# Kernel tuning notes

Hardware: AMD Instinct MI355X
Metric: run time of the kernel (lower is better)

The kernel has to match this reference:

```python
import jax, jax.numpy as jnp
import numpy as np

EPS = 1e-7      # GENConv message epsilon
BN_EPS = 1e-5   # torch BatchNorm1d eps


def _genconv(x, src, dst, n, w1, b1, gamma, beta, w2, b2):
    # GENConv(aggr='softmax_sg', t=1.0): msg = relu(x_j)+eps, per-feature
    # scatter-softmax weights (stop-grad), weighted sum, residual, MLP
    # [Linear -> BatchNorm(train stats) -> ReLU -> Linear].
    msg = jnp.maximum(x[src], 0.0) + EPS                         # [E, d]
    m = jax.ops.segment_max(msg, dst, num_segments=n)            # [N, d]
    e = jnp.exp(msg - m[dst])
    s = jax.ops.segment_sum(e, dst, num_segments=n)
    alpha = jax.lax.stop_gradient(e / (s[dst] + 1e-16))          # softmax_sg
    agg = jax.ops.segment_sum(msg * alpha, dst, num_segments=n)  # [N, d]
    h = agg + x
    h = h @ w1 + b1
    mu = jnp.mean(h, axis=0)
    var = jnp.var(h, axis=0)
    h = (h - mu) * jax.lax.rsqrt(var + BN_EPS) * gamma + beta
    h = jnp.maximum(h, 0.0)
    return h @ w2 + b2


def _forward(x, edge_index, batch, target,
             g1_w1, g1_b1, g1_g, g1_be, g1_w2, g1_b2,
             g2_w1, g2_b1, g2_g, g2_be, g2_w2, g2_b2,
             g3_w1, g3_b1, g3_g, g3_be, g3_w2, g3_b2,
             fg1_w, fg1_b, fg2_w, fg2_b, fg3_w, fg3_b,
             emb, cw, cb, fxt_w, fxt_b,
             f1_w, f1_b, f2_w, f2_b, o_w, o_b):
    n = x.shape[0]
    nb = target.shape[0]
    src, dst = edge_index[0], edge_index[1]
    h = jnp.maximum(_genconv(x, src, dst, n, g1_w1, g1_b1, g1_g, g1_be, g1_w2, g1_b2), 0.0)
    h = jnp.maximum(_genconv(h, src, dst, n, g2_w1, g2_b1, g2_g, g2_be, g2_w2, g2_b2), 0.0)
    h = jnp.maximum(_genconv(h, src, dst, n, g3_w1, g3_b1, g3_g, g3_be, g3_w2, g3_b2), 0.0)
    # global mean pool over graphs
    sums = jax.ops.segment_sum(h, batch, num_segments=nb)
    cnt = jax.ops.segment_sum(jnp.ones((n, 1), h.dtype), batch, num_segments=nb)
    xg = sums / jnp.maximum(cnt, 1.0)
    xg = jnp.maximum(xg @ fg1_w + fg1_b, 0.0)
    xg = jnp.maximum(xg @ fg2_w + fg2_b, 0.0)
    xg = jnp.maximum(xg @ fg3_w + fg3_b, 0.0)
    # protein branch: embed [B,1000,128], Conv1d(1000->32,k=8) over embed axis
    ext = emb[target]                                            # [B, 1000, 128]
    conv = jax.lax.conv_general_dilated(
        ext, cw, (1,), 'VALID',
        dimension_numbers=('NCW', 'OIW', 'NCW')) + cb[None, :, None]  # [B, 32, 121]
    xt = conv.reshape(nb, 32 * 121) @ fxt_w + fxt_b
    xc = jnp.concatenate([xg, xt], axis=1)                       # [B, 256]
    xc = jnp.maximum(xc @ f1_w + f1_b, 0.0)
    xc = jnp.maximum(xc @ f2_w + f2_b, 0.0)
    return xc @ o_w + o_b


def _lin(k, i, o):
    kw, kb = jax.random.split(k)
    s = 1.0 / np.sqrt(i)
    return (jax.random.uniform(kw, (i, o), jnp.float32, -s, s),
            jax.random.uniform(kb, (o,), jnp.float32, -s, s))


def setup_inputs():
    key = jax.random.key(0)
    ks = jax.random.split(key, 32)
    N, E, B, D = 30000, 150000, 256, 78
    d = {}
    d['x'] = jax.random.normal(ks[0], (N, D), jnp.float32)
    d['edge_index'] = jax.random.randint(ks[1], (2, E), 0, N)
    d['batch'] = jnp.sort(jax.random.randint(ks[2], (N,), 0, B))
    d['target'] = jax.random.randint(ks[3], (B, 1000), 0, 26)
    dims = [(78, 156, 78), (78, 156, 312), (312, 624, 624)]
    for li, (i, hdim, o) in enumerate(dims, start=1):
        w1, b1 = _lin(ks[4 + 2 * li], i, hdim)
        w2, b2 = _lin(ks[5 + 2 * li], hdim, o)
        d['g%d_w1' % li], d['g%d_b1' % li] = w1, b1
        d['g%d_g' % li] = jnp.ones((hdim,), jnp.float32)
        d['g%d_be' % li] = jnp.zeros((hdim,), jnp.float32)
        d['g%d_w2' % li], d['g%d_b2' % li] = w2, b2
    d['fg1_w'], d['fg1_b'] = _lin(ks[14], 624, 512)
    d['fg2_w'], d['fg2_b'] = _lin(ks[15], 512, 1024)
    d['fg3_w'], d['fg3_b'] = _lin(ks[16], 1024, 128)
    d['emb'] = jax.random.normal(ks[17], (26, 128), jnp.float32)
    s = 1.0 / np.sqrt(1000 * 8)
    d['cw'] = jax.random.uniform(ks[18], (32, 1000, 8), jnp.float32, -s, s)
    d['cb'] = jax.random.uniform(ks[19], (32,), jnp.float32, -s, s)
    d['fxt_w'], d['fxt_b'] = _lin(ks[20], 32 * 121, 128)
    d['f1_w'], d['f1_b'] = _lin(ks[21], 256, 1024)
    d['f2_w'], d['f2_b'] = _lin(ks[22], 1024, 512)
    d['o_w'], d['o_b'] = _lin(ks[23], 512, 1)
    return d


def reference(x, edge_index, batch, target,
              g1_w1, g1_b1, g1_g, g1_be, g1_w2, g1_b2,
              g2_w1, g2_b1, g2_g, g2_be, g2_w2, g2_b2,
              g3_w1, g3_b1, g3_g, g3_be, g3_w2, g3_b2,
              fg1_w, fg1_b, fg2_w, fg2_b, fg3_w, fg3_b,
              emb, cw, cb, fxt_w, fxt_b,
              f1_w, f1_b, f2_w, f2_b, o_w, o_b):
    return _forward(x, edge_index, batch, target,
                    g1_w1, g1_b1, g1_g, g1_be, g1_w2, g1_b2,
                    g2_w1, g2_b1, g2_g, g2_be, g2_w2, g2_b2,
                    g3_w1, g3_b1, g3_g, g3_be, g3_w2, g3_b2,
                    fg1_w, fg1_b, fg2_w, fg2_b, fg3_w, fg3_b,
                    emb, cw, cb, fxt_w, fxt_b,
                    f1_w, f1_b, f2_w, f2_b, o_w, o_b)
```

## Files before the change

### kernel.cpp

```cpp
#include <hip/hip_runtime.h>
#include <hip/hip_bf16.h>

typedef unsigned short u16;
typedef __attribute__((ext_vector_type(8))) short bh8;
typedef __attribute__((ext_vector_type(4))) float f32x4;

static __device__ __forceinline__ float b2fu(u16 u) {
    union { float f; unsigned int i; } x;
    x.i = ((unsigned int)u) << 16;
    return x.f;
}
static __device__ __forceinline__ u16 f2bu(float f) {
    __hip_bfloat16 h = __float2bfloat16(f);
    union { __hip_bfloat16 h; u16 u; } x;
    x.h = h;
    return x.u;
}
static __device__ __forceinline__ void load2(const float* p, float& v0, float& v1) {
    float2 v = *reinterpret_cast<const float2*>(p);
    v0 = v.x; v1 = v.y;
}
static __device__ __forceinline__ void load2(const u16* p, float& v0, float& v1) {
    unsigned int u = *reinterpret_cast<const unsigned int*>(p);
    v0 = b2fu((u16)(u & 0xffff)); v1 = b2fu((u16)(u >> 16));
}

static __device__ __forceinline__ void gload16(const u16* g, u16* l) {
    __builtin_amdgcn_global_load_lds(
        (const __attribute__((address_space(1))) unsigned int*)(const void*)g,
        (__attribute__((address_space(3))) unsigned int*)(void*)l, 16, 0, 0);
}


__global__ __launch_bounds__(256) void const_out_kernel(float* __restrict__ out, float v, int n) {
    int i = blockIdx.x * 256 + threadIdx.x;
    if (i < n) out[i] = v;
}


__global__ __launch_bounds__(256) void hist_kernel(const int* __restrict__ dst,
                                                   int* __restrict__ hist, int E) {
    int e = blockIdx.x * 256 + threadIdx.x;
    if (e < E) atomicAdd(&hist[dst[e]], 1);
}

__global__ __launch_bounds__(256) void scan_kernel(const int* __restrict__ hist,
                                                   int* __restrict__ rowptr,
                                                   int* __restrict__ fill, int N) {
    __shared__ int csum[256];
    __shared__ int coff[257];
    int t = threadIdx.x;
    int chunk = (N + 255) / 256;
    int lo = min(t * chunk, N), hi = min(lo + chunk, N);
    int s = 0;
    for (int i = lo; i < hi; i++) s += hist[i];
    csum[t] = s;
    __syncthreads();
    if (t == 0) {
        int acc = 0;
        for (int i = 0; i < 256; i++) { coff[i] = acc; acc += csum[i]; }
        rowptr[N] = acc;
    }
    __syncthreads();
    int run = coff[t];
    for (int i = lo; i < hi; i++) {
        rowptr[i] = run;
        fill[i] = run;
        run += hist[i];
    }
}

__global__ __launch_bounds__(256) void scan_tiles(const int* __restrict__ hist, int N,
                                                  int* __restrict__ rowptr,
                                                  int* __restrict__ tsum) {
    int tid = threadIdx.x;
    int i = blockIdx.x * 256 + tid;
    int v = (i < N) ? hist[i] : 0;
    __shared__ int s[256];
    s[tid] = v;
    __syncthreads();
    for (int off = 1; off < 256; off <<= 1) {
        int t = (tid >= off) ? s[tid - off] : 0;
        __syncthreads();
        s[tid] += t;
        __syncthreads();
    }
    if (i < N) rowptr[i] = s[tid] - v;
    if (tid == 255) tsum[blockIdx.x] = s[255];
}

__global__ __launch_bounds__(256) void scan_tsum(const int* __restrict__ tsum, int ntiles,
                                                 int* __restrict__ toff,
                                                 int* __restrict__ totalp) {
    int tid = threadIdx.x;
    int v = (tid < ntiles) ? tsum[tid] : 0;
    __shared__ int s[256];
    s[tid] = v;
    __syncthreads();
    for (int off = 1; off < 256; off <<= 1) {
        int t = (tid >= off) ? s[tid - off] : 0;
        __syncthreads();
        s[tid] += t;
        __syncthreads();
    }
    if (tid < ntiles) toff[tid] = s[tid] - v;
    if (tid == 255) *totalp = s[255];
}

__global__ __launch_bounds__(256) void scan_apply(int* __restrict__ rowptr,
                                                  const int* __restrict__ toff, int N,
                                                  int* __restrict__ fill) {
    int i = blockIdx.x * 256 + threadIdx.x;
    if (i < N) {
        int r = rowptr[i] + toff[blockIdx.x];
        rowptr[i] = r;
        fill[i] = r;
    }
}

__global__ __launch_bounds__(256) void scatter_kernel(const int* __restrict__ src,
                                                      const int* __restrict__ dst,
                                                      int* __restrict__ fill,
                                                      int* __restrict__ srcs, int E) {
    int e = blockIdx.x * 256 + threadIdx.x;
    if (e < E) {
        int p = atomicAdd(&fill[dst[e]], 1);
        srcs[p] = src[e];
    }
}


template <typename T>
__global__ __launch_bounds__(256) void agg_kernel(const T* __restrict__ x,
                                                  const int* __restrict__ rowptr,
                                                  const int* __restrict__ srcs,
                                                  u16* __restrict__ out, int d, int Kp, int N) {
    int n = blockIdx.y * 4 + (threadIdx.x >> 6);
    int f = (blockIdx.x * 64 + (threadIdx.x & 63)) * 2;
    if (n >= N || f >= Kp) return;
    size_t o = (size_t)n * Kp + f;
    if (f >= d) {
        *reinterpret_cast<unsigned int*>(out + o) = 0;
        return;
    }
    int e0 = rowptr[n], e1 = rowptr[n + 1];
    float s0 = 0.f, t0 = 0.f, s1 = 0.f, t1 = 0.f;
    for (int e = e0; e < e1; e++) {
        int sr = srcs[e];
        float v0, v1;
        load2(x + (size_t)sr * d + f, v0, v1);
        float m0 = fmaxf(v0, 0.f) + 1e-7f;
        float w0 = __expf(m0);
        s0 += w0; t0 += m0 * w0;
        float m1 = fmaxf(v1, 0.f) + 1e-7f;
        float w1 = __expf(m1);
        s1 += w1; t1 += m1 * w1;
    }
    float x0, x1;
    load2(x + (size_t)n * d + f, x0, x1);
    float a0 = t0 / (s0 + 1e-16f) + x0;
    float a1 = t1 / (s1 + 1e-16f) + x1;
    unsigned int pk = (unsigned int)f2bu(a0) | ((unsigned int)f2bu(a1) << 16);
    *reinterpret_cast<unsigned int*>(out + o) = pk;
}


__global__ __launch_bounds__(256) void wt_cvt(const float* __restrict__ W, int K, int N,
                                              u16* __restrict__ WT, int Kp, int Np) {
    int n = blockIdx.y * 4 + (threadIdx.x >> 6);
    int k = blockIdx.x * 64 + (threadIdx.x & 63);
    if (n >= Np || k >= Kp) return;
    float v = (n < N && k < K) ? W[(size_t)k * N + n] : 0.f;
    WT[(size_t)n * Kp + k] = f2bu(v);
}


__global__ __launch_bounds__(256) void cvt_bn(const u16* __restrict__ H,
                                              const float* __restrict__ scale,
                                              const float* __restrict__ shift,
                                              u16* __restrict__ out, int dh, int Kp, int M) {
    int m = blockIdx.y * 4 + (threadIdx.x >> 6);
    int f = blockIdx.x * 64 + (threadIdx.x & 63);
    if (m >= M || f >= Kp) return;
    size_t o = (size_t)m * Kp + f;
    if (f >= dh) { out[o] = 0; return; }
    float v = fmaxf(fmaf(b2fu(H[(size_t)m * dh + f]), scale[f], shift[f]), 0.f);
    out[o] = f2bu(v);
}


template <bool RELU, typename CT>
__global__ __launch_bounds__(256) void gemm_mfma(const u16* __restrict__ A,
                                                 const u16* __restrict__ BT,
                                                 const float* __restrict__ bias,
                                                 CT* __restrict__ C, int ldc, int M, int Ncols,
                                                 int Kp, int nbx, int nby, int spx) {
    int xcd = blockIdx.x & 7;
    int j = blockIdx.x >> 3;
    int bx = j % nbx;
    int by = xcd * spx + j / nbx;
    if (by >= nby) return;
    __shared__ u16 As[2][128 * 32];
    __shared__ u16 Bs[2][128 * 32];
    const int tid = threadIdx.x;
    const int lane = tid & 63;
    const int w = tid >> 6;
    const int bm = by * 128;
    const int bn = bx * 128;
    f32x4 acc[4][4] = {};

    const int r0 = w * 16 + (lane >> 2);
    const int r1 = r0 + 64;
    const int sw = ((lane & 3) ^ ((r0 >> 1) & 3)) << 3;
    const u16* Ag0 = A + (size_t)(bm + r0) * Kp + sw;
    const u16* Ag1 = A + (size_t)(bm + r1) * Kp + sw;
    const u16* Bg0 = BT + (size_t)(bn + r0) * Kp + sw;
    const u16* Bg1 = BT + (size_t)(bn + r1) * Kp + sw;
    const int wb = w << 9;

    auto stage = [&](int b, int koff) {
        gload16(Ag0 + koff, &As[b][wb]);
        gload16(Ag1 + koff, &As[b][2048 + wb]);
        gload16(Bg0 + koff, &Bs[b][wb]);
        gload16(Bg1 + koff, &Bs[b][2048 + wb]);
    };

    const int fm = (w >> 1) * 64 + (lane & 15);
    const int fn = (w & 1) * 64 + (lane & 15);
    const int g = lane >> 4;
    const int ka = (g ^ ((fm >> 1) & 3)) << 3;
    const int kb = (g ^ ((fn >> 1) & 3)) << 3;

    const int nk = Kp >> 5;
    stage(0, 0);
    asm volatile("s_waitcnt vmcnt(0)" ::: "memory");
    __builtin_amdgcn_s_barrier();
    for (int k = 0; k < nk; k++) {
        const int cur = k & 1;
        if (k + 1 < nk) stage(cur ^ 1, (k + 1) << 5);
        bh8 af[4], bf[4];
#pragma unroll
        for (int mt = 0; mt < 4; mt++)
            af[mt] = *reinterpret_cast<const bh8*>(&As[cur][(fm + mt * 16) * 32 + ka]);
#pragma unroll
        for (int nt = 0; nt < 4; nt++)
            bf[nt] = *reinterpret_cast<const bh8*>(&Bs[cur][(fn + nt * 16) * 32 + kb]);
        asm volatile("s_waitcnt lgkmcnt(0)" ::: "memory");
        __builtin_amdgcn_sched_barrier(0);
        __builtin_amdgcn_s_setprio(1);
#pragma unroll
        for (int mt = 0; mt < 4; mt++)
#pragma unroll
            for (int nt = 0; nt < 4; nt++)
                acc[mt][nt] = __builtin_amdgcn_mfma_f32_16x16x32_bf16(af[mt], bf[nt],
                                                                      acc[mt][nt], 0, 0, 0);
        __builtin_amdgcn_s_setprio(0);
        __builtin_amdgcn_sched_barrier(0);
        asm volatile("s_waitcnt vmcnt(0)" ::: "memory");
        __builtin_amdgcn_s_barrier();
    }
    const int rq = (lane >> 4) * 4;
    const int cl = lane & 15;
#pragma unroll
    for (int mt = 0; mt < 4; mt++) {
#pragma unroll
        for (int nt = 0; nt < 4; nt++) {
            int n = bn + (w & 1) * 64 + nt * 16 + cl;
            if (n >= Ncols) continue;
            float bv = bias[n];
#pragma unroll
            for (int r = 0; r < 4; r++) {
                int m = bm + (w >> 1) * 64 + mt * 16 + rq + r;
                if (m >= M) continue;
                float v = acc[mt][nt][r] + bv;
                if (RELU) v = fmaxf(v, 0.f);
                if (sizeof(CT) == 2)
                    C[(size_t)m * ldc + n] = (CT)f2bu(v);
                else
                    C[(size_t)m * ldc + n] = (CT)v;
            }
        }
    }
}


__global__ __launch_bounds__(256) void bn_stats(const u16* __restrict__ H, int N, int dh,
                                                float* __restrict__ sum,
                                                float* __restrict__ sumsq) {
    int col = blockIdx.x * 64 + (threadIdx.x & 63);
    int rl = threadIdx.x >> 6;
    int rowsPerBlock = (N + gridDim.y - 1) / gridDim.y;
    int r0 = blockIdx.y * rowsPerBlock;
    int r1 = min(r0 + rowsPerBlock, N);
    float s0 = 0.f, s1 = 0.f;
    if (col < dh) {
        for (int r = r0 + rl; r < r1; r += 4) {
            float v = b2fu(H[(size_t)r * dh + col]);
            s0 += v;
            s1 += v * v;
        }
    }
    __shared__ float ls0[4][64];
    __shared__ float ls1[4][64];
    ls0[rl][threadIdx.x & 63] = s0;
    ls1[rl][threadIdx.x & 63] = s1;
    __syncthreads();
    if (rl == 0 && col < dh) {
        int c = threadIdx.x & 63;
        atomicAdd(&sum[col], ls0[0][c] + ls0[1][c] + ls0[2][c] + ls0[3][c]);
        atomicAdd(&sumsq[col], ls1[0][c] + ls1[1][c] + ls1[2][c] + ls1[3][c]);
    }
}

__global__ __launch_bounds__(256) void bn_final(const float* __restrict__ sum,
                                                const float* __restrict__ sumsq,
                                                const float* __restrict__ gamma,
                                                const float* __restrict__ beta,
                                                float* __restrict__ scale,
                                                float* __restrict__ shift, int dh, float invN) {
    int i = blockIdx.x * 256 + threadIdx.x;
    if (i < dh) {
        float mu = sum[i] * invN;
        float var = sumsq[i] * invN - mu * mu;
        float sc = gamma[i] / sqrtf(var + 1e-5f);
        scale[i] = sc;
        shift[i] = beta[i] - mu * sc;
    }
}


__global__ __launch_bounds__(256) void pool_seg(const u16* __restrict__ h,
                                                const int* __restrict__ goff,
                                                float* __restrict__ gsum, int d) {
    int g = blockIdx.y;
    int c = threadIdx.x & 63;
    int f = blockIdx.x * 64 + c;
    int wv = threadIdx.x >> 6;
    int r0 = goff[g], r1 = goff[g + 1];
    float s = 0.f;
    if (f < d)
        for (int r = r0 + wv; r < r1; r += 4) s += b2fu(h[(size_t)r * d + f]);
    __shared__ float ls[4][64];
    ls[wv][c] = s;
    __syncthreads();
    if (wv == 0 && f < d) {
        float tot = ls[0][c] + ls[1][c] + ls[2][c] + ls[3][c];
        gsum[(size_t)g * d + f] = tot / fmaxf((float)(r1 - r0), 1.f);
    }
}


__global__ __launch_bounds__(256) void gemm_sk(const float* __restrict__ A, int lda,
                                               const float* __restrict__ B, int ldb,
                                               float* __restrict__ C, int ldc, int M, int K,
                                               int Nn, int KC) {
    __shared__ float As[16][17];
    __shared__ float Bs[16][68];
    const int tid = threadIdx.x;
    const int bn = blockIdx.x * 64;
    const int bm = blockIdx.y * 16;
    const int k0 = blockIdx.z * KC;
    const int kend = min(K, k0 + KC);
    const int tx = tid & 63;
    const int ty = tid >> 6;
    float acc[4] = {};
    const int am = bm + (tid >> 4);
    const int ak = tid & 15;
    for (int kk0 = k0; kk0 < kend; kk0 += 16) {
        {
            int k = kk0 + ak;
            As[ak][tid >> 4] = (am < M && k < kend) ? A[(size_t)am * lda + k] : 0.f;
        }
#pragma unroll
        for (int i = 0; i < 4; i++) {
            int k = kk0 + ty + 4 * i;
            Bs[ty + 4 * i][tx] = (k < kend && bn + tx < Nn) ? B[(size_t)k * ldb + bn + tx] : 0.f;
        }
        __syncthreads();
#pragma unroll
        for (int kk = 0; kk < 16; kk++) {
            float b = Bs[kk][tx];
#pragma unroll
            for (int i = 0; i < 4; i++) acc[i] = fmaf(As[kk][ty + 4 * i], b, acc[i]);
        }
        __syncthreads();
    }
    if (bn + tx < Nn) {
#pragma unroll
        for (int i = 0; i < 4; i++) {
            int m = bm + ty + 4 * i;
            if (m < M) atomicAdd(&C[(size_t)m * ldc + bn + tx], acc[i]);
        }
    }
}

__global__ __launch_bounds__(256) void bias_act(float* __restrict__ C, int ldc,
                                                const float* __restrict__ bias, int M, int Nn,
                                                int relu) {
    int idx = blockIdx.x * 256 + threadIdx.x;
    if (idx >= M * Nn) return;
    int m = idx / Nn, n = idx - m * Nn;
    float v = C[(size_t)m * ldc + n] + bias[n];
    C[(size_t)m * ldc + n] = relu ? fmaxf(v, 0.f) : v;
}

static void launch_gemm_small(const float* A, int lda, const float* B, int ldb,
                              const float* bias, float* C, int ldc, int M, int K, int Nn,
                              bool relu, hipStream_t stream) {
    int gx = (Nn + 63) / 64, gy = (M + 15) / 16;
    int tiles = gx * gy;
    int ksplit = 512 / tiles;
    if (ksplit < 1) ksplit = 1;
    int maxsplit = (K + 63) / 64;
    if (ksplit > maxsplit) ksplit = maxsplit;
    int KC = (((K + ksplit - 1) / ksplit) + 15) & ~15;
    ksplit = (K + KC - 1) / KC;
    gemm_sk<<<dim3(gx, gy, ksplit), 256, 0, stream>>>(A, lda, B, ldb, C, ldc, M, K, Nn, KC);
    bias_act<<<(M * Nn + 255) / 256, 256, 0, stream>>>(C, ldc, bias, M, Nn, relu ? 1 : 0);
}


__global__ __launch_bounds__(256) void hone_kernel(const int* __restrict__ target,
                                                   u16* __restrict__ H, int total) {
    int i = blockIdx.x * 256 + threadIdx.x;
    if (i >= total) return;
    int b = i / 1000, pos = i - b * 1000;
    int t = target[i];
    H[((size_t)b * 26 + t) * 1024 + pos] = 0x3F80;
}

__global__ __launch_bounds__(256) void cwt_cvt(const float* __restrict__ cw,
                                               u16* __restrict__ BT) {
    int n = blockIdx.y;
    int kk = blockIdx.x * 256 + threadIdx.x;
    int o = n >> 3, k = n & 7;
    float v = (kk < 1000) ? cw[(size_t)o * 8000 + (size_t)kk * 8 + k] : 0.f;
    BT[(size_t)n * 1024 + kk] = f2bu(v);
}

__global__ __launch_bounds__(256) void prot_conv_kernel(const float* __restrict__ S,
                                                        const float* __restrict__ emb,
                                                        const float* __restrict__ cb,
                                                        float* __restrict__ out) {
    int b = blockIdx.x;
    int tid = threadIdx.x;
    __shared__ float Sl[6656];
    __shared__ float el[26 * 128];
    for (int i = tid; i < 6656; i += 256) Sl[i] = S[(size_t)b * 6656 + i];
    for (int i = tid; i < 26 * 128; i += 256) el[i] = emb[i];
    __syncthreads();
    for (int j = tid; j < 3872; j += 256) {
        int o = j / 121;
        int w = j - o * 121;
        float acc = cb[o];
        for (int t = 0; t < 26; t++) {
#pragma unroll
            for (int k = 0; k < 8; k++)
                acc = fmaf(Sl[t * 256 + o * 8 + k], el[t * 128 + w + k], acc);
        }
        out[(size_t)b * 3872 + j] = acc;
    }
}


__global__ __launch_bounds__(256) void out_kernel(const float* __restrict__ A,
                                                  const float* __restrict__ w,
                                                  const float* __restrict__ bias,
                                                  float* __restrict__ out, int M, int K) {
    int wave = threadIdx.x >> 6;
    int lane = threadIdx.x & 63;
    int r = blockIdx.x * 4 + wave;
    if (r >= M) return;
    float acc = 0.f;
    for (int k = lane; k < K; k += 64) acc += A[(size_t)r * K + k] * w[k];
    for (int off = 32; off > 0; off >>= 1) acc += __shfl_down(acc, off, 64);
    if (lane == 0) out[r] = acc + bias[0];
}


static inline int KP(int k) { return (k + 31) & ~31; }
static inline int NP(int n) { return (n + 127) & ~127; }

extern "C" void kernel_launch(void* const* d_in, const int* in_sizes, int n_in, void* d_out,
                              int out_size, void* d_ws, size_t ws_size, hipStream_t stream) {
    static const int exp_sizes[39] = {
        2340000, 300000, 30000, 256000,
        12168, 156, 156, 156, 12168, 78,
        12168, 156, 156, 156, 48672, 312,
        194688, 624, 624, 624, 389376, 624,
        319488, 512, 524288, 1024, 131072, 128,
        3328, 256000, 32, 495616, 128,
        262144, 1024, 524288, 512, 512, 1};
    int bad = (n_in != 39) ? 100 : -1;
    if (bad < 0)
        for (int i = 0; i < 39; i++)
            if (in_sizes[i] != exp_sizes[i]) { bad = i; break; }
    if (bad >= 0) {
        const_out_kernel<<<1, 256, 0, stream>>>((float*)d_out, 2048.f + 8.f * bad, out_size);
        return;
    }

    const int N = 30000, E = 150000, B = 256;
    const int Mp = 30080;
    const int nby = 235, spx = 30;
    const int ntiles = (N + 255) / 256;
    const float* x_in = (const float*)d_in[0];
    const int* ei = (const int*)d_in[1];
    const int* src = ei;
    const int* dst = ei + E;
    const int* batch = (const int*)d_in[2];
    const int* target = (const int*)d_in[3];

    char* p = (char*)d_ws;
    auto carve = [&](size_t bytes) {
        char* r = p;
        p += (bytes + 15) & ~(size_t)15;
        return r;
    };
    int* hist = (int*)carve((size_t)(N + B) * 4);
    int* ghist = hist + N;
    int* rowptr = (int*)carve((size_t)(N + 1) * 4);
    int* fill = (int*)carve((size_t)N * 4);
    int* srcs = (int*)carve((size_t)E * 4);
    int* goff = (int*)carve((size_t)(B + 1) * 4);
    int* gfill = (int*)carve((size_t)B * 4);
    int* tsum = (int*)carve(256 * 4);
    int* toff = (int*)carve(256 * 4);
    float* sum_ = (float*)carve(2 * 624 * 4);
    float* sumsq_ = sum_ + 624;
    float* scale_ = (float*)carve(624 * 4);
    float* shift_ = (float*)carve(624 * 4);
    float* zero256 = (float*)carve(256 * 4);
    float* gsum = (float*)carve((size_t)B * 624 * 4);
    float* fc1 = (float*)carve((size_t)B * 512 * 4);
    float* fc2 = (float*)carve((size_t)B * 1024 * 4);
    float* xc = (float*)carve((size_t)B * 256 * 4);
    float* fcc1 = (float*)carve((size_t)B * 1024 * 4);
    float* fcc2 = (float*)carve((size_t)B * 512 * 4);
    float* Sbuf = (float*)carve((size_t)B * 6656 * 4);
    float* convb = (float*)carve((size_t)B * 3872 * 4);
    u16* Hbuf = (u16*)carve((size_t)B * 26 * 1024 * 2);
    u16* cwT = (u16*)carve((size_t)256 * 1024 * 2);
    u16* Abf = (u16*)carve((size_t)Mp * 640 * 2);
    u16* hmidb = (u16*)carve((size_t)N * 624 * 2);
    u16* Lout = (u16*)carve((size_t)N * 624 * 2);
    struct Layer { int di, dh, dn, w1, b1, g, be, w2, b2; };
    const Layer L[3] = {
        {78, 156, 78, 4, 5, 6, 7, 8, 9},
        {78, 156, 312, 10, 11, 12, 13, 14, 15},
        {312, 624, 624, 16, 17, 18, 19, 20, 21},
    };
    u16* WT1[3];
    u16* WT2[3];
    for (int li = 0; li < 3; li++) {
        WT1[li] = (u16*)carve((size_t)NP(L[li].dh) * KP(L[li].di) * 2);
        WT2[li] = (u16*)carve((size_t)NP(L[li].dn) * KP(L[li].dh) * 2);
    }
    size_t need = (size_t)(p - (char*)d_ws);
    if (ws_size < need) {
        const_out_kernel<<<1, 256, 0, stream>>>((float*)d_out,
                                                1024.f + (float)(ws_size >> 20), out_size);
        return;
    }

    hipMemsetAsync(hist, 0, (size_t)(N + B) * 4, stream);
    hipMemsetAsync(zero256, 0, 256 * 4, stream);
    hist_kernel<<<(E + 255) / 256, 256, 0, stream>>>(dst, hist, E);
    hist_kernel<<<(N + 255) / 256, 256, 0, stream>>>(batch, ghist, N);
    scan_tiles<<<ntiles, 256, 0, stream>>>(hist, N, rowptr, tsum);
    scan_tsum<<<1, 256, 0, stream>>>(tsum, ntiles, toff, rowptr + N);
    scan_apply<<<ntiles, 256, 0, stream>>>(rowptr, toff, N, fill);
    scan_kernel<<<1, 256, 0, stream>>>(ghist, goff, gfill, B);
    scatter_kernel<<<(E + 255) / 256, 256, 0, stream>>>(src, dst, fill, srcs, E);

    for (int li = 0; li < 3; li++) {
        int Kp1 = KP(L[li].di), Np1 = NP(L[li].dh);
        int Kp2 = KP(L[li].dh), Np2 = NP(L[li].dn);
        wt_cvt<<<dim3((Kp1 + 63) / 64, Np1 / 4), 256, 0, stream>>>(
            (const float*)d_in[L[li].w1], L[li].di, L[li].dh, WT1[li], Kp1, Np1);
        wt_cvt<<<dim3((Kp2 + 63) / 64, Np2 / 4), 256, 0, stream>>>(
            (const float*)d_in[L[li].w2], L[li].dh, L[li].dn, WT2[li], Kp2, Np2);
    }

    for (int li = 0; li < 3; li++) {
        const int di = L[li].di, dh = L[li].dh, dn = L[li].dn;
        const int Kp1 = KP(di), Kp2 = KP(dh);
        if (li == 0)
            agg_kernel<float><<<dim3((Kp1 / 2 + 63) / 64, (N + 3) / 4), 256, 0, stream>>>(
                x_in, rowptr, srcs, Abf, di, Kp1, N);
        else
            agg_kernel<u16><<<dim3((Kp1 / 2 + 63) / 64, (N + 3) / 4), 256, 0, stream>>>(
                Lout, rowptr, srcs, Abf, di, Kp1, N);
        {
            int nbx = NP(dh) / 128;
            gemm_mfma<false, u16><<<dim3(8 * spx * nbx), 256, 0, stream>>>(
                Abf, WT1[li], (const float*)d_in[L[li].b1], hmidb, dh, N, dh, Kp1, nbx, nby,
                spx);
        }
        hipMemsetAsync(sum_, 0, 2 * 624 * 4, stream);
        bn_stats<<<dim3((dh + 63) / 64, 60), 256, 0, stream>>>(hmidb, N, dh, sum_, sumsq_);
        bn_final<<<(dh + 255) / 256, 256, 0, stream>>>(sum_, sumsq_, (const float*)d_in[L[li].g],
                                                       (const float*)d_in[L[li].be], scale_,
                                                       shift_, dh, 1.0f / N);
        cvt_bn<<<dim3((Kp2 + 63) / 64, (N + 3) / 4), 256, 0, stream>>>(hmidb, scale_, shift_,
                                                                       Abf, dh, Kp2, N);
        {
            int nbx = NP(dn) / 128;
            gemm_mfma<true, u16><<<dim3(8 * spx * nbx), 256, 0, stream>>>(
                Abf, WT2[li], (const float*)d_in[L[li].b2], Lout, dn, N, dn, Kp2, nbx, nby,
                spx);
        }
    }

    pool_seg<<<dim3(10, B), 256, 0, stream>>>(Lout, goff, gsum, 624);

    hipMemsetAsync(fc1, 0, (size_t)B * 3328 * 4, stream);

    launch_gemm_small(gsum, 624, (const float*)d_in[22], 512, (const float*)d_in[23], fc1, 512,
                      B, 624, 512, true, stream);
    launch_gemm_small(fc1, 512, (const float*)d_in[24], 1024, (const float*)d_in[25], fc2, 1024,
                      B, 512, 1024, true, stream);
    launch_gemm_small(fc2, 1024, (const float*)d_in[26], 128, (const float*)d_in[27], xc, 256,
                      B, 1024, 128, true, stream);

    hipMemsetAsync(Hbuf, 0, (size_t)B * 26 * 1024 * 2, stream);
    hone_kernel<<<(B * 1000 + 255) / 256, 256, 0, stream>>>(target, Hbuf, B * 1000);
    cwt_cvt<<<dim3(4, 256), 256, 0, stream>>>((const float*)d_in[29], cwT);
    {
        int nbxS = 2, nbyS = 52, spxS = 7;
        gemm_mfma<false, float><<<dim3(8 * spxS * nbxS), 256, 0, stream>>>(
            Hbuf, cwT, zero256, Sbuf, 256, 6656, 256, 1024, nbxS, nbyS, spxS);
    }
    prot_conv_kernel<<<B, 256, 0, stream>>>(Sbuf, (const float*)d_in[28],
                                            (const float*)d_in[30], convb);
    launch_gemm_small(convb, 3872, (const float*)d_in[31], 128, (const float*)d_in[32],
                      xc + 128, 256, B, 3872, 128, false, stream);

    launch_gemm_small(xc, 256, (const float*)d_in[33], 1024, (const float*)d_in[34], fcc1, 1024,
                      B, 256, 1024, true, stream);
    launch_gemm_small(fcc1, 1024, (const float*)d_in[35], 512, (const float*)d_in[36], fcc2, 512,
                      B, 1024, 512, true, stream);
    out_kernel<<<(B + 3) / 4, 256, 0, stream>>>(fcc2, (const float*)d_in[37],
                                                (const float*)d_in[38], (float*)d_out, B, 512);
}
```

Measured before the change: 927.2 us.

## Fuse BatchNorm stats into GEMM1 epilogue and BN-apply into GEMM2 A-load

The first MLP GEMM now accumulates per-column sum and sum-of-squares in its epilogue, reduced through LDS and then atomically added to global buffers. The second GEMM loads A through registers and applies the BN scale/shift and ReLU before writing to LDS. This removes the separate bn_stats and cvt_bn kernels and their extra passes over the hidden activations. In exchange the GEMM2 A path loses its async direct-to-LDS load, adds VALU work and register pressure, and the global atomics per block increase.

After: 798.8 us. -13.8%, faster.

```diff
diff --git a/kernel.cpp b/kernel.cpp
--- a/kernel.cpp
+++ b/kernel.cpp
@@ -175,26 +175,16 @@
 }
 
 
-__global__ __launch_bounds__(256) void cvt_bn(const u16* __restrict__ H,
-                                              const float* __restrict__ scale,
-                                              const float* __restrict__ shift,
-                                              u16* __restrict__ out, int dh, int Kp, int M) {
-    int m = blockIdx.y * 4 + (threadIdx.x >> 6);
-    int f = blockIdx.x * 64 + (threadIdx.x & 63);
-    if (m >= M || f >= Kp) return;
-    size_t o = (size_t)m * Kp + f;
-    if (f >= dh) { out[o] = 0; return; }
-    float v = fmaxf(fmaf(b2fu(H[(size_t)m * dh + f]), scale[f], shift[f]), 0.f);
-    out[o] = f2bu(v);
-}
-
-
-template <bool RELU, typename CT>
+template <int AMODE, int EMODE, bool RELU, typename CT>
 __global__ __launch_bounds__(256) void gemm_mfma(const u16* __restrict__ A,
                                                  const u16* __restrict__ BT,
                                                  const float* __restrict__ bias,
                                                  CT* __restrict__ C, int ldc, int M, int Ncols,
-                                                 int Kp, int nbx, int nby, int spx) {
+                                                 int Kp, int nbx, int nby, int spx,
+                                                 const float* __restrict__ scale,
+                                                 const float* __restrict__ shift,
+                                                 float* __restrict__ osum,
+                                                 float* __restrict__ osumsq) {
     int xcd = blockIdx.x & 7;
     int j = blockIdx.x >> 3;
     int bx = j % nbx;
@@ -218,11 +208,42 @@
     const u16* Bg1 = BT + (size_t)(bn + r1) * Kp + sw;
     const int wb = w << 9;
 
-    auto stage = [&](int b, int koff) {
+    uint4 a0r, a1r;
+    auto stageB = [&](int b, int koff) {
+        gload16(Bg0 + koff, &Bs[b][wb]);
+        gload16(Bg1 + koff, &Bs[b][2048 + wb]);
+    };
+    auto stageA_lds = [&](int b, int koff) {
         gload16(Ag0 + koff, &As[b][wb]);
         gload16(Ag1 + koff, &As[b][2048 + wb]);
-        gload16(Bg0 + koff, &Bs[b][wb]);
-        gload16(Bg1 + koff, &Bs[b][2048 + wb]);
+    };
+    auto loadA_reg = [&](int koff) {
+        a0r = *reinterpret_cast<const uint4*>(Ag0 + koff);
+        a1r = *reinterpret_cast<const uint4*>(Ag1 + koff);
+    };
+    auto writeA_reg = [&](int b, int koff) {
+        int f0 = sw + koff;
+        float4 sc0 = *reinterpret_cast<const float4*>(scale + f0);
+        float4 sc1 = *reinterpret_cast<const float4*>(scale + f0 + 4);
+        float4 sh0 = *reinterpret_cast<const float4*>(shift + f0);
+        float4 sh1 = *reinterpret_cast<const float4*>(shift + f0 + 4);
+        auto tf2 = [](unsigned int u, float sa, float sb, float ha, float hb) {
+            float h0 = b2fu((u16)(u & 0xffff)), h1 = b2fu((u16)(u >> 16));
+            float v0 = fmaxf(fmaf(h0, sa, ha), 0.f);
+            float v1 = fmaxf(fmaf(h1, sb, hb), 0.f);
+            return (unsigned int)f2bu(v0) | ((unsigned int)f2bu(v1) << 16);
+        };
+        uint4 o0, o1;
+        o0.x = tf2(a0r.x, sc0.x, sc0.y, sh0.x, sh0.y);
+        o0.y = tf2(a0r.y, sc0.z, sc0.w, sh0.z, sh0.w);
+        o0.z = tf2(a0r.z, sc1.x, sc1.y, sh1.x, sh1.y);
+        o0.w = tf2(a0r.w, sc1.z, sc1.w, sh1.z, sh1.w);
+        o1.x = tf2(a1r.x, sc0.x, sc0.y, sh0.x, sh0.y);
+        o1.y = tf2(a1r.y, sc0.z, sc0.w, sh0.z, sh0.w);
+        o1.z = tf2(a1r.z, sc1.x, sc1.y, sh1.x, sh1.y);
+        o1.w = tf2(a1r.w, sc1.z, sc1.w, sh1.z, sh1.w);
+        *reinterpret_cast<uint4*>(&As[b][wb + lane * 8]) = o0;
+        *reinterpret_cast<uint4*>(&As[b][2048 + wb + lane * 8]) = o1;
     };
 
     const int fm = (w >> 1) * 64 + (lane & 15);
@@ -232,12 +253,25 @@
     const int kb = (g ^ ((fn >> 1) & 3)) << 3;
 
     const int nk = Kp >> 5;
-    stage(0, 0);
-    asm volatile("s_waitcnt vmcnt(0)" ::: "memory");
+    if constexpr (AMODE == 0) {
+        stageA_lds(0, 0);
+        stageB(0, 0);
+        asm volatile("s_waitcnt vmcnt(0)" ::: "memory");
+    } else {
+        loadA_reg(0);
+        stageB(0, 0);
+        asm volatile("s_waitcnt vmcnt(0)" ::: "memory");
+        writeA_reg(0, 0);
+        asm volatile("s_waitcnt lgkmcnt(0)" ::: "memory");
+    }
     __builtin_amdgcn_s_barrier();
     for (int k = 0; k < nk; k++) {
         const int cur = k & 1;
-        if (k + 1 < nk) stage(cur ^ 1, (k + 1) << 5);
+        if (k + 1 < nk) {
+            if constexpr (AMODE == 0) stageA_lds(cur ^ 1, (k + 1) << 5);
+            else loadA_reg((k + 1) << 5);
+            stageB(cur ^ 1, (k + 1) << 5);
+        }
         bh8 af[4], bf[4];
 #pragma unroll
         for (int mt = 0; mt < 4; mt++)
@@ -257,74 +291,102 @@
         __builtin_amdgcn_s_setprio(0);
         __builtin_amdgcn_sched_barrier(0);
         asm volatile("s_waitcnt vmcnt(0)" ::: "memory");
+        if constexpr (AMODE == 1) {
+            __builtin_amdgcn_sched_barrier(0);
+            if (k + 1 < nk) writeA_reg(cur ^ 1, (k + 1) << 5);
+            asm volatile("s_waitcnt lgkmcnt(0)" ::: "memory");
+        }
         __builtin_amdgcn_s_barrier();
     }
     const int rq = (lane >> 4) * 4;
     const int cl = lane & 15;
-#pragma unroll
-    for (int mt = 0; mt < 4; mt++) {
+    if constexpr (EMODE == 0) {
+#pragma unroll
+        for (int mt = 0; mt < 4; mt++) {
+#pragma unroll
+            for (int nt = 0; nt < 4; nt++) {
+                int n = bn + (w & 1) * 64 + nt * 16 + cl;
+                if (n >= Ncols) continue;
+                float bv = bias[n];
+#pragma unroll
+                for (int r = 0; r < 4; r++) {
+                    int m = bm + (w >> 1) * 64 + mt * 16 + rq + r;
+                    if (m >= M) continue;
+                    float v = acc[mt][nt][r] + bv;
+                    if (RELU) v = fmaxf(v, 0.f);
+                    if (sizeof(CT) == 2)
+                        C[(size_t)m * ldc + n] = (CT)f2bu(v);
+                    else
+                        C[(size_t)m * ldc + n] = (CT)v;
+                }
+            }
+        }
+    } else {
+        float cs[4] = {0.f, 0.f, 0.f, 0.f}, cq[4] = {0.f, 0.f, 0.f, 0.f};
 #pragma unroll
         for (int nt = 0; nt < 4; nt++) {
             int n = bn + (w & 1) * 64 + nt * 16 + cl;
-            if (n >= Ncols) continue;
-            float bv = bias[n];
-#pragma unroll
-            for (int r = 0; r < 4; r++) {
-                int m = bm + (w >> 1) * 64 + mt * 16 + rq + r;
-                if (m >= M) continue;
-                float v = acc[mt][nt][r] + bv;
-                if (RELU) v = fmaxf(v, 0.f);
-                if (sizeof(CT) == 2)
-                    C[(size_t)m * ldc + n] = (CT)f2bu(v);
-                else
-                    C[(size_t)m * ldc + n] = (CT)v;
+            if (n >= ldc) continue;
+            float bv = (n < Ncols) ? bias[n] : 0.f;
+#pragma unroll
+            for (int mt = 0; mt < 4; mt++) {
+#pragma unroll
+                for (int r = 0; r < 4; r++) {
+                    int m = bm + (w >> 1) * 64 + mt * 16 + rq + r;
+                    if (m >= M) continue;
+                    float v = (n < Ncols) ? acc[mt][nt][r] + bv : 0.f;
+                    u16 vb = f2bu(v);
+                    C[(size_t)m * ldc + n] = (CT)vb;
+                    float vf = b2fu(vb);
+                    cs[nt] += vf;
+                    cq[nt] += vf * vf;
+                }
             }
         }
-    }
-}
-
-
-__global__ __launch_bounds__(256) void bn_stats(const u16* __restrict__ H, int N, int dh,
-                                                float* __restrict__ sum,
-                                                float* __restrict__ sumsq) {
-    int col = blockIdx.x * 64 + (threadIdx.x & 63);
-    int rl = threadIdx.x >> 6;
-    int rowsPerBlock = (N + gridDim.y - 1) / gridDim.y;
-    int r0 = blockIdx.y * rowsPerBlock;
-    int r1 = min(r0 + rowsPerBlock, N);
-    float s0 = 0.f, s1 = 0.f;
-    if (col < dh) {
-        for (int r = r0 + rl; r < r1; r += 4) {
-            float v = b2fu(H[(size_t)r * dh + col]);
-            s0 += v;
-            s1 += v * v;
-        }
-    }
-    __shared__ float ls0[4][64];
-    __shared__ float ls1[4][64];
-    ls0[rl][threadIdx.x & 63] = s0;
-    ls1[rl][threadIdx.x & 63] = s1;
-    __syncthreads();
-    if (rl == 0 && col < dh) {
-        int c = threadIdx.x & 63;
-        atomicAdd(&sum[col], ls0[0][c] + ls0[1][c] + ls0[2][c] + ls0[3][c]);
-        atomicAdd(&sumsq[col], ls1[0][c] + ls1[1][c] + ls1[2][c] + ls1[3][c]);
-    }
-}
+        float* red = (float*)&As[0][0];
+        const int slot = (w >> 1) * 4 + (lane >> 4);
+#pragma unroll
+        for (int nt = 0; nt < 4; nt++) {
+            int nl = (w & 1) * 64 + nt * 16 + cl;
+            red[nl * 8 + slot] = cs[nt];
+            red[1024 + nl * 8 + slot] = cq[nt];
+        }
+        __syncthreads();
+        if (tid < 128) {
+            int n = bn + tid;
+            if (n < Ncols) {
+                float s = 0.f, q = 0.f;
+#pragma unroll
+                for (int i = 0; i < 8; i++) {
+                    s += red[tid * 8 + i];
+                    q += red[1024 + tid * 8 + i];
+                }
+                atomicAdd(&osum[n], s);
+                atomicAdd(&osumsq[n], q);
+            }
+        }
+    }
+}
+
 
 __global__ __launch_bounds__(256) void bn_final(const float* __restrict__ sum,
                                                 const float* __restrict__ sumsq,
                                                 const float* __restrict__ gamma,
                                                 const float* __restrict__ beta,
                                                 float* __restrict__ scale,
-                                                float* __restrict__ shift, int dh, float invN) {
+                                                float* __restrict__ shift, int dh, int Kp,
+                                                float invN) {
     int i = blockIdx.x * 256 + threadIdx.x;
+    if (i >= Kp) return;
     if (i < dh) {
         float mu = sum[i] * invN;
         float var = sumsq[i] * invN - mu * mu;
         float sc = gamma[i] / sqrtf(var + 1e-5f);
         scale[i] = sc;
         shift[i] = beta[i] - mu * sc;
+    } else {
+        scale[i] = 0.f;
+        shift[i] = 0.f;
     }
 }
 
@@ -528,8 +590,8 @@
     int* toff = (int*)carve(256 * 4);
     float* sum_ = (float*)carve(2 * 624 * 4);
     float* sumsq_ = sum_ + 624;
-    float* scale_ = (float*)carve(624 * 4);
-    float* shift_ = (float*)carve(624 * 4);
+    float* scale_ = (float*)carve(640 * 4);
+    float* shift_ = (float*)carve(640 * 4);
     float* zero256 = (float*)carve(256 * 4);
     float* gsum = (float*)carve((size_t)B * 624 * 4);
     float* fc1 = (float*)carve((size_t)B * 512 * 4);
@@ -542,7 +604,7 @@
     u16* Hbuf = (u16*)carve((size_t)B * 26 * 1024 * 2);
     u16* cwT = (u16*)carve((size_t)256 * 1024 * 2);
     u16* Abf = (u16*)carve((size_t)Mp * 640 * 2);
-    u16* hmidb = (u16*)carve((size_t)N * 624 * 2);
+    u16* hmidb = (u16*)carve((size_t)Mp * 640 * 2);
     u16* Lout = (u16*)carve((size_t)N * 624 * 2);
     struct Layer { int di, dh, dn, w1, b1, g, be, w2, b2; };
     const Layer L[3] = {
@@ -591,24 +653,21 @@
         else
             agg_kernel<u16><<<dim3((Kp1 / 2 + 63) / 64, (N + 3) / 4), 256, 0, stream>>>(
                 Lout, rowptr, srcs, Abf, di, Kp1, N);
+        hipMemsetAsync(sum_, 0, 2 * 624 * 4, stream);
         {
             int nbx = NP(dh) / 128;
-            gemm_mfma<false, u16><<<dim3(8 * spx * nbx), 256, 0, stream>>>(
-                Abf, WT1[li], (const float*)d_in[L[li].b1], hmidb, dh, N, dh, Kp1, nbx, nby,
-                spx);
-        }
-        hipMemsetAsync(sum_, 0, 2 * 624 * 4, stream);
-        bn_stats<<<dim3((dh + 63) / 64, 60), 256, 0, stream>>>(hmidb, N, dh, sum_, sumsq_);
-        bn_final<<<(dh + 255) / 256, 256, 0, stream>>>(sum_, sumsq_, (const float*)d_in[L[li].g],
-                                                       (const float*)d_in[L[li].be], scale_,
-                                                       shift_, dh, 1.0f / N);
-        cvt_bn<<<dim3((Kp2 + 63) / 64, (N + 3) / 4), 256, 0, stream>>>(hmidb, scale_, shift_,
-                                                                       Abf, dh, Kp2, N);
+            gemm_mfma<0, 1, false, u16><<<dim3(8 * spx * nbx), 256, 0, stream>>>(
+                Abf, WT1[li], (const float*)d_in[L[li].b1], hmidb, Kp2, N, dh, Kp1, nbx, nby,
+                spx, nullptr, nullptr, sum_, sumsq_);
+        }
+        bn_final<<<(Kp2 + 255) / 256, 256, 0, stream>>>(
+            sum_, sumsq_, (const float*)d_in[L[li].g], (const float*)d_in[L[li].be], scale_,
+            shift_, dh, Kp2, 1.0f / N);
         {
             int nbx = NP(dn) / 128;
-            gemm_mfma<true, u16><<<dim3(8 * spx * nbx), 256, 0, stream>>>(
-                Abf, WT2[li], (const float*)d_in[L[li].b2], Lout, dn, N, dn, Kp2, nbx, nby,
-                spx);
+            gemm_mfma<1, 0, true, u16><<<dim3(8 * spx * nbx), 256, 0, stream>>>(
+                hmidb, WT2[li], (const float*)d_in[L[li].b2], Lout, dn, N, dn, Kp2, nbx, nby,
+                spx, scale_, shift_, nullptr, nullptr);
         }
     }
 
@@ -628,8 +687,9 @@
     cwt_cvt<<<dim3(4, 256), 256, 0, stream>>>((const float*)d_in[29], cwT);
     {
         int nbxS = 2, nbyS = 52, spxS = 7;
-        gemm_mfma<false, float><<<dim3(8 * spxS * nbxS), 256, 0, stream>>>(
-            Hbuf, cwT, zero256, Sbuf, 256, 6656, 256, 1024, nbxS, nbyS, spxS);
+        gemm_mfma<0, 0, false, float><<<dim3(8 * spxS * nbxS), 256, 0, stream>>>(
+            Hbuf, cwT, zero256, Sbuf, 256, 6656, 256, 1024, nbxS, nbyS, spxS, nullptr, nullptr,
+            nullptr, nullptr);
     }
     prot_conv_kernel<<<B, 256, 0, stream>>>(Sbuf, (const float*)d_in[28],
                                             (const float*)d_in[30], convb);
```
